# Performance work log

Hardware: AMD Instinct MI355X
Metric: run time of the kernel (lower is better)

Reference implementation:

```python
import jax, jax.numpy as jnp
import numpy as np

ALIBI_SLOPES = jnp.array([0.6299605249, 0.396850263, 0.25, 0.1574901312,
                          0.0992125657, 0.0625, 0.0393725328, 0.0248031414,
                          0.015625, 0.0098431332, 0.0062007854, 0.00390625],
                         dtype=jnp.float32)
H, D = 12, 64
SCALE = D ** (-0.5)


def setup_inputs() -> dict:
    key = jax.random.key(0)
    ks = jax.random.split(key, 9)
    B, S, E = 4, 2048, 768
    s = 0.02
    return {
        "x": jax.random.normal(ks[0], (B, S, E), dtype=jnp.float32),
        "Wq": jax.random.normal(ks[1], (E, E), dtype=jnp.float32) * s,
        "bq": jnp.zeros((E,), dtype=jnp.float32),
        "Wk": jax.random.normal(ks[2], (E, E), dtype=jnp.float32) * s,
        "bk": jnp.zeros((E,), dtype=jnp.float32),
        "Wv": jax.random.normal(ks[3], (E, E), dtype=jnp.float32) * s,
        "bv": jnp.zeros((E,), dtype=jnp.float32),
        "Wo": jax.random.normal(ks[4], (E, E), dtype=jnp.float32) * s,
        "bo": jnp.zeros((E,), dtype=jnp.float32),
    }


def reference(x, Wq, bq, Wk, bk, Wv, bv, Wo, bo):
    B, S, E = x.shape
    # projections (weights stored input-major: y = x @ W + b)
    q = (x @ Wq + bq).reshape(B, S, H, D).transpose(0, 2, 1, 3)  # [B,H,S,D]
    k = (x @ Wk + bk).reshape(B, S, H, D).transpose(0, 2, 1, 3)
    v = (x @ Wv + bv).reshape(B, S, H, D).transpose(0, 2, 1, 3)

    scores = jnp.einsum('bhqd,bhkd->bhqk', q, k) * SCALE  # [B,H,S,S]

    pos = jnp.arange(S, dtype=jnp.float32)
    a = ALIBI_SLOPES[:, None] * pos[None, :]          # [H,S]
    alibi = a[:, :, None] - a[:, None, :]             # [H,S,S]
    scores = scores + alibi[None]

    causal = jnp.triu(jnp.ones((S, S), dtype=bool), k=1)  # True above diag
    scores = jnp.where(causal[None, None], -jnp.inf, scores)

    attn = jax.nn.softmax(scores, axis=-1)
    o = jnp.einsum('bhqk,bhkd->bhqd', attn, v)  # [B,H,S,D]

    # Faithful to original: view of contiguous (B,H,S,D) buffer as (B,S,E)
    # (head-major flatten, reproducing the original module's reshape).
    o = o.reshape(B, S, E)
    return o @ Wo + bo
```

## Files before the change

### kernel.cpp

```cpp
#include <hip/hip_runtime.h>
#include <hip/hip_bf16.h>
#include <cstdint>
#include <cstddef>

#define B_ 4
#define S_ 2048
#define E_ 768
#define H_ 12
#define D_ 64

typedef __bf16 bf16x8 __attribute__((ext_vector_type(8)));
typedef float f32x4 __attribute__((ext_vector_type(4)));

__constant__ float c_slopes[12] = {
    0.6299605249f, 0.396850263f, 0.25f, 0.1574901312f,
    0.0992125657f, 0.0625f, 0.0393725328f, 0.0248031414f,
    0.015625f, 0.0098431332f, 0.0062007854f, 0.00390625f};

__device__ __forceinline__ unsigned short f2bf_u(float f) {
    unsigned u = __builtin_bit_cast(unsigned, f);
    u += 0x7fffu + ((u >> 16) & 1u);
    return (unsigned short)(u >> 16);
}
__device__ __forceinline__ __bf16 f2bf(float f) {
    unsigned short s = f2bf_u(f);
    return __builtin_bit_cast(__bf16, s);
}

__device__ __forceinline__ void gload_lds16(const void* g, void* l) {
    __builtin_amdgcn_global_load_lds(
        (const __attribute__((address_space(1))) unsigned int*)g,
        (__attribute__((address_space(3))) unsigned int*)l, 16, 0, 0);
}

__global__ __launch_bounds__(256) void cvt_x(const float* __restrict__ src,
                                             __bf16* __restrict__ dst) {
    int i = (blockIdx.x * 256 + threadIdx.x) * 4;
    float4 v = *(const float4*)(src + i);
    ushort4 o;
    o.x = f2bf_u(v.x); o.y = f2bf_u(v.y); o.z = f2bf_u(v.z); o.w = f2bf_u(v.w);
    *(ushort4*)((unsigned short*)dst + i) = o;
}

__global__ __launch_bounds__(256) void wtrans(const float* __restrict__ W0,
                                              const float* __restrict__ W1,
                                              const float* __restrict__ W2,
                                              const float* __restrict__ W3,
                                              __bf16* __restrict__ Wt) {
    const float* W = blockIdx.z == 0 ? W0 : blockIdx.z == 1 ? W1
                   : blockIdx.z == 2 ? W2 : W3;
    __bf16* out = Wt + (size_t)blockIdx.z * E_ * E_;
    __shared__ alignas(16) __bf16 ts[64 * 72];
    const int t = threadIdx.x;
    const int k0 = blockIdx.y * 64, n0 = blockIdx.x * 64;
#pragma unroll
    for (int i = 0; i < 4; i++) {
        int idx = i * 256 + t;
        int row = idx >> 4, c4 = idx & 15;
        float4 v = *(const float4*)(W + (size_t)(k0 + row) * E_ + n0 + c4 * 4);
        ts[(c4 * 4 + 0) * 72 + row] = f2bf(v.x);
        ts[(c4 * 4 + 1) * 72 + row] = f2bf(v.y);
        ts[(c4 * 4 + 2) * 72 + row] = f2bf(v.z);
        ts[(c4 * 4 + 3) * 72 + row] = f2bf(v.w);
    }
    __syncthreads();
#pragma unroll
    for (int i = 0; i < 2; i++) {
        int idx = i * 256 + t;
        int r = idx >> 3, c8 = idx & 7;
        *(uint4*)((unsigned short*)out + (size_t)(n0 + r) * E_ + k0 + c8 * 8) =
            *(const uint4*)((const unsigned short*)ts + r * 72 + c8 * 8);
    }
}

__global__ __launch_bounds__(256, 3) void qkv_gemm(
    const __bf16* __restrict__ A, const __bf16* __restrict__ WtAll,
    const float* __restrict__ b0, const float* __restrict__ b1,
    const float* __restrict__ b2, __bf16* __restrict__ Qb,
    __bf16* __restrict__ Kb, __bf16* __restrict__ Vtb) {
    constexpr int Kd = E_;
    __shared__ alignas(16) __bf16 Asm[2][128 * 32];
    __shared__ alignas(16) __bf16 Bsm[2][3][64 * 32];

    const int t = threadIdx.x;
    const int w = t >> 6, lane = t & 63;
    const int qm = lane & 15, quad = lane >> 4;
    const int m0 = blockIdx.y * 128, n0 = blockIdx.x * 64;
    const int wm = w * 32;

    float bvv[3][4];
    const float* bs[3] = {b0, b1, b2};
#pragma unroll
    for (int z = 0; z < 3; z++)
#pragma unroll
        for (int j = 0; j < 4; j++) bvv[z][j] = bs[z][n0 + j * 16 + qm];

    const int crow = lane >> 2;
    const int ccol = lane & 3;

    f32x4 acc[3][2][4] = {};

    for (int k0 = 0; k0 < Kd; k0 += 64) {
#pragma unroll
        for (int p = 0; p < 2; p++) {
            const int kp = k0 + p * 32;
#pragma unroll
            for (int cc = 0; cc < 2; cc++) {
                int chunk = w * 2 + cc;
                gload_lds16((const unsigned short*)A +
                                (size_t)(m0 + chunk * 16 + crow) * Kd + kp + ccol * 8,
                            Asm[p] + chunk * 512);
            }
#pragma unroll
            for (int e = 0; e < 3; e++) {
                int g = w * 3 + e;
                int z = g >> 2, cz = g & 3;
                gload_lds16((const unsigned short*)WtAll + (size_t)z * Kd * E_ +
                                (size_t)(n0 + cz * 16 + crow) * Kd + kp + ccol * 8,
                            Bsm[p][z] + cz * 512);
            }
        }
        __syncthreads();

#pragma unroll
        for (int p = 0; p < 2; p++) {
            bf16x8 af[2];
#pragma unroll
            for (int i = 0; i < 2; i++)
                af[i] = *(const bf16x8*)(Asm[p] + (wm + i * 16 + qm) * 32 + quad * 8);
#pragma unroll
            for (int z = 0; z < 3; z++) {
                bf16x8 bg[4];
#pragma unroll
                for (int j = 0; j < 4; j++)
                    bg[j] = *(const bf16x8*)(Bsm[p][z] + (j * 16 + qm) * 32 + quad * 8);
#pragma unroll
                for (int i = 0; i < 2; i++)
#pragma unroll
                    for (int j = 0; j < 4; j++)
                        acc[z][i][j] = __builtin_amdgcn_mfma_f32_16x16x32_bf16(
                            af[i], bg[j], acc[z][i][j], 0, 0, 0);
            }
        }
        __syncthreads();
    }

#pragma unroll
    for (int z = 0; z < 3; z++) {
        __bf16* out = z == 0 ? Qb : z == 1 ? Kb : Vtb;
#pragma unroll
        for (int i = 0; i < 2; i++) {
#pragma unroll
            for (int j = 0; j < 4; j++) {
                int col = n0 + j * 16 + qm;
                int rowb = m0 + wm + i * 16 + quad * 4;
                int h = col >> 6, d = col & (D_ - 1);
                if (z == 2) {
                    int b = rowb >> 11, s = rowb & (S_ - 1);
                    unsigned short pk4[4];
#pragma unroll
                    for (int r = 0; r < 4; r++)
                        pk4[r] = f2bf_u(acc[z][i][j][r] + bvv[z][j]);
                    uint2 pv;
                    pv.x = (unsigned)pk4[0] | ((unsigned)pk4[1] << 16);
                    pv.y = (unsigned)pk4[2] | ((unsigned)pk4[3] << 16);
                    *(uint2*)((unsigned short*)out +
                              ((size_t)(b * H_ + h) * D_ + d) * S_ + s) = pv;
                } else {
#pragma unroll
                    for (int r = 0; r < 4; r++) {
                        int row = rowb + r;
                        int b = row >> 11, s = row & (S_ - 1);
                        out[(((size_t)(b * H_ + h)) * S_ + s) * D_ + d] =
                            f2bf(acc[z][i][j][r] + bvv[z][j]);
                    }
                }
            }
        }
    }
}

__global__ __launch_bounds__(256) void gemm_out(
    const __bf16* __restrict__ A, const __bf16* __restrict__ Wt,
    const float* __restrict__ bias, float* __restrict__ outF) {
    constexpr int Kd = E_, N = E_;
    __shared__ alignas(16) __bf16 Asm[2][128 * 32];
    __shared__ alignas(16) __bf16 Bsm[2][128 * 32];

    const int t = threadIdx.x;
    const int w = t >> 6, lane = t & 63;
    const int qm = lane & 15, quad = lane >> 4;
    const int m0 = blockIdx.y * 128, n0 = blockIdx.x * 128;
    const int wm = (w >> 1) * 64, wn = (w & 1) * 64;

    float bvv[4];
#pragma unroll
    for (int j = 0; j < 4; j++) bvv[j] = bias[n0 + wn + j * 16 + qm];

    const int crow = lane >> 2;
    const int ccol = lane & 3;

    f32x4 acc[4][4] = {};

    for (int k0 = 0; k0 < Kd; k0 += 64) {
#pragma unroll
        for (int p = 0; p < 2; p++) {
            const int kp = k0 + p * 32;
#pragma unroll
            for (int cc = 0; cc < 2; cc++) {
                int chunk = w * 2 + cc;
                int row = chunk * 16 + crow;
                gload_lds16((const unsigned short*)A + (size_t)(m0 + row) * Kd + kp + ccol * 8,
                            Asm[p] + chunk * 512);
                gload_lds16((const unsigned short*)Wt + (size_t)(n0 + row) * Kd + kp + ccol * 8,
                            Bsm[p] + chunk * 512);
            }
        }
        __syncthreads();

#pragma unroll
        for (int p = 0; p < 2; p++) {
            bf16x8 af[4], bg[4];
#pragma unroll
            for (int i = 0; i < 4; i++)
                af[i] = *(const bf16x8*)(Asm[p] + (wm + i * 16 + qm) * 32 + quad * 8);
#pragma unroll
            for (int j = 0; j < 4; j++)
                bg[j] = *(const bf16x8*)(Bsm[p] + (wn + j * 16 + qm) * 32 + quad * 8);
#pragma unroll
            for (int i = 0; i < 4; i++)
#pragma unroll
                for (int j = 0; j < 4; j++)
                    acc[i][j] = __builtin_amdgcn_mfma_f32_16x16x32_bf16(
                        af[i], bg[j], acc[i][j], 0, 0, 0);
        }
        __syncthreads();
    }

#pragma unroll
    for (int i = 0; i < 4; i++) {
#pragma unroll
        for (int j = 0; j < 4; j++) {
            int col = n0 + wn + j * 16 + qm;
            int rowb = m0 + wm + i * 16 + quad * 4;
#pragma unroll
            for (int r = 0; r < 4; r++) {
                int row = rowb + r;
                outF[(size_t)row * N + col] = acc[i][j][r] + bvv[j];
            }
        }
    }
}

__global__ __launch_bounds__(256, 6) void attn_k(
    const __bf16* __restrict__ Q, const __bf16* __restrict__ K,
    const __bf16* __restrict__ Vt, __bf16* __restrict__ O) {
    __shared__ alignas(16) __bf16 Ksm[2][64 * 32];
    __shared__ alignas(16) __bf16 Vsm[2][64 * 32];
    __shared__ alignas(16) __bf16 Psm[4 * 16 * 64];

    const int t = threadIdx.x;
    const int w = t >> 6, lane = t & 63;
    const int qm = lane & 15, quad = lane >> 4;
    const int L = blockIdx.x;
    const int r = L & 7;
    const int m = (L >> 3) & 31;
    const int s = L >> 8;
    const int bh = r * 6 + s;
    const int qt = (m + s * 5 + (s >> 1)) & 31;
    const float c2 = c_slopes[bh % H_] * 1.44269504f;
    const size_t base = (size_t)bh * S_ * D_;

    const int bb = qt * 64 + w * 16;
    const __bf16* qp = Q + base + (size_t)(bb + qm) * D_ + quad * 8;
    bf16x8 qf0 = *(const bf16x8*)qp;
    bf16x8 qf1 = *(const bf16x8*)(qp + 32);

    f32x4 oacc[4] = {};
    float lsum = 0.f;
    char* Pb = (char*)Psm + w * 2048;

    const int srow = lane >> 2;
    const int sq = (lane & 3) ^ ((lane >> 3) & 3);
    const unsigned short* Kg = (const unsigned short*)K + base +
                               (size_t)(16 * w + srow) * D_ + sq * 8;
    const unsigned short* Vg = (const unsigned short*)Vt + base +
                               (size_t)(16 * w + srow) * S_ + sq * 8;

    const int cq = (quad ^ ((qm >> 1) & 3)) * 8;
    const int pf = (qm & 7) << 4;

    for (int kt = 0; kt <= qt; kt++) {
#pragma unroll
        for (int h = 0; h < 2; h++) {
            gload_lds16(Kg + (size_t)(kt * 64) * D_ + 32 * h, Ksm[h] + w * 512);
            gload_lds16(Vg + kt * 64 + 32 * h, Vsm[h] + w * 512);
        }
        __syncthreads();

        bf16x8 ak[4][2], bv[4][2];
#pragma unroll
        for (int i = 0; i < 4; i++) {
            ak[i][0] = *(const bf16x8*)(Ksm[0] + (16 * i + qm) * 32 + cq);
            ak[i][1] = *(const bf16x8*)(Ksm[1] + (16 * i + qm) * 32 + cq);
        }
#pragma unroll
        for (int jd = 0; jd < 4; jd++) {
            bv[jd][0] = *(const bf16x8*)(Vsm[0] + (16 * jd + qm) * 32 + cq);
            bv[jd][1] = *(const bf16x8*)(Vsm[1] + (16 * jd + qm) * 32 + cq);
        }

        f32x4 st[4];
#pragma unroll
        for (int i = 0; i < 4; i++) {
            f32x4 zz = {0.f, 0.f, 0.f, 0.f};
            zz = __builtin_amdgcn_mfma_f32_16x16x32_bf16(ak[i][0], qf0, zz, 0, 0, 0);
            zz = __builtin_amdgcn_mfma_f32_16x16x32_bf16(ak[i][1], qf1, zz, 0, 0, 0);
            st[i] = zz;
        }

        const int qi = bb + qm;
        const bool nomask = (kt * 64 + 63) <= bb;
        float ls = 0.f;
        unsigned pk[4][2];
#pragma unroll
        for (int i = 0; i < 4; i++) {
            float bi = -c2 * (float)(kt * 64 + 16 * i + 4 * quad);
            float p[4];
#pragma unroll
            for (int rr = 0; rr < 4; rr++) {
                float tt = st[i][rr] * 0.18033688f + (bi - c2 * (float)rr);
                float pp = __builtin_amdgcn_exp2f(tt);
                if (!nomask) {
                    int key = kt * 64 + 16 * i + 4 * quad + rr;
                    pp = (key > qi) ? 0.f : pp;
                }
                ls += pp;
                p[rr] = pp;
            }
            unsigned u0 = __builtin_bit_cast(unsigned, p[0]) + 0x8000u;
            unsigned u1 = __builtin_bit_cast(unsigned, p[1]) + 0x8000u;
            unsigned u2 = __builtin_bit_cast(unsigned, p[2]) + 0x8000u;
            unsigned u3 = __builtin_bit_cast(unsigned, p[3]) + 0x8000u;
            pk[i][0] = __builtin_amdgcn_perm(u1, u0, 0x07060302u);
            pk[i][1] = __builtin_amdgcn_perm(u3, u2, 0x07060302u);
        }
        lsum += ls;

#pragma unroll
        for (int i = 0; i < 4; i++) {
            uint2 pv; pv.x = pk[i][0]; pv.y = pk[i][1];
            *(uint2*)(Pb + qm * 128 + ((32 * i + 8 * quad) ^ pf)) = pv;
        }

        bf16x8 ap0 = *(const bf16x8*)(Pb + qm * 128 + ((quad * 16) ^ pf));
        bf16x8 ap1 = *(const bf16x8*)(Pb + qm * 128 + ((64 + quad * 16) ^ pf));
#pragma unroll
        for (int jd = 0; jd < 4; jd++) {
            oacc[jd] = __builtin_amdgcn_mfma_f32_16x16x32_bf16(
                ap0, bv[jd][0], oacc[jd], 0, 0, 0);
            oacc[jd] = __builtin_amdgcn_mfma_f32_16x16x32_bf16(
                ap1, bv[jd][1], oacc[jd], 0, 0, 0);
        }

        __syncthreads();
    }

    float lf = lsum;
    lf += __shfl_xor(lf, 16);
    lf += __shfl_xor(lf, 32);
#pragma unroll
    for (int rr = 0; rr < 4; rr++) {
        float lr = __shfl(lf, 4 * quad + rr);
        float inv = 1.0f / lr;
        int qrow = bb + 4 * quad + rr;
#pragma unroll
        for (int jd = 0; jd < 4; jd++)
            O[base + (size_t)qrow * D_ + 16 * jd + qm] =
                f2bf(oacc[jd][rr] * inv);
    }
}

extern "C" void kernel_launch(void* const* d_in, const int* in_sizes, int n_in,
                              void* d_out, int out_size, void* d_ws, size_t ws_size,
                              hipStream_t stream) {
    (void)in_sizes; (void)n_in; (void)out_size; (void)ws_size;
    const float* x  = (const float*)d_in[0];
    const float* Wq = (const float*)d_in[1];
    const float* bq = (const float*)d_in[2];
    const float* Wk = (const float*)d_in[3];
    const float* bk = (const float*)d_in[4];
    const float* Wv = (const float*)d_in[5];
    const float* bv = (const float*)d_in[6];
    const float* Wo = (const float*)d_in[7];
    const float* bo = (const float*)d_in[8];
    float* out = (float*)d_out;

    const size_t n = (size_t)B_ * H_ * S_ * D_;
    __bf16* xb  = (__bf16*)d_ws;
    __bf16* Qb  = xb + n;
    __bf16* Kb  = xb + 2 * n;
    __bf16* Vtb = xb + 3 * n;
    __bf16* Wt  = xb + 4 * n;
    __bf16* Ob  = Qb;

    cvt_x<<<6144, 256, 0, stream>>>(x, xb);
    wtrans<<<dim3(12, 12, 4), 256, 0, stream>>>(Wq, Wk, Wv, Wo, Wt);
    qkv_gemm<<<dim3(12, 64), 256, 0, stream>>>(
        xb, Wt, bq, bk, bv, Qb, Kb, Vtb);
    attn_k<<<1536, 256, 0, stream>>>(Qb, Kb, Vtb, Ob);
    gemm_out<<<dim3(6, 64), 256, 0, stream>>>(
        Ob, Wt + 3 * (size_t)E_ * E_, bo, out);
}
```

Measured before the change: 218.8 us.

## Merge input conversion kernels and shrink output GEMM tile to 128x64

Folds the x-to-bf16 conversion and weight transpose into one launch, dispatching on block index, which removes one kernel launch and the gap between the two. The output projection GEMM moves from 128x128 to 128x64 tiles, doubling the grid from 384 to 768 blocks and adding an occupancy hint, to fill more of the GPU's compute units. Smaller tiles reuse less data per block and reload the A operand more often.

```diff
diff --git a/kernel.cpp b/kernel.cpp
--- a/kernel.cpp
+++ b/kernel.cpp
@@ -33,26 +33,27 @@
         (__attribute__((address_space(3))) unsigned int*)l, 16, 0, 0);
 }
 
-__global__ __launch_bounds__(256) void cvt_x(const float* __restrict__ src,
-                                             __bf16* __restrict__ dst) {
-    int i = (blockIdx.x * 256 + threadIdx.x) * 4;
-    float4 v = *(const float4*)(src + i);
-    ushort4 o;
-    o.x = f2bf_u(v.x); o.y = f2bf_u(v.y); o.z = f2bf_u(v.z); o.w = f2bf_u(v.w);
-    *(ushort4*)((unsigned short*)dst + i) = o;
-}
-
-__global__ __launch_bounds__(256) void wtrans(const float* __restrict__ W0,
-                                              const float* __restrict__ W1,
-                                              const float* __restrict__ W2,
-                                              const float* __restrict__ W3,
-                                              __bf16* __restrict__ Wt) {
-    const float* W = blockIdx.z == 0 ? W0 : blockIdx.z == 1 ? W1
-                   : blockIdx.z == 2 ? W2 : W3;
-    __bf16* out = Wt + (size_t)blockIdx.z * E_ * E_;
+__global__ __launch_bounds__(256) void prep(
+    const float* __restrict__ x, __bf16* __restrict__ xb,
+    const float* __restrict__ W0, const float* __restrict__ W1,
+    const float* __restrict__ W2, const float* __restrict__ W3,
+    __bf16* __restrict__ Wt) {
     __shared__ alignas(16) __bf16 ts[64 * 72];
+    const int L = blockIdx.x;
     const int t = threadIdx.x;
-    const int k0 = blockIdx.y * 64, n0 = blockIdx.x * 64;
+    if (L < 6144) {
+        int i = (L * 256 + t) * 4;
+        float4 v = *(const float4*)(x + i);
+        ushort4 o;
+        o.x = f2bf_u(v.x); o.y = f2bf_u(v.y); o.z = f2bf_u(v.z); o.w = f2bf_u(v.w);
+        *(ushort4*)((unsigned short*)xb + i) = o;
+        return;
+    }
+    const int id = L - 6144;
+    const int z = id / 144, rem = id % 144;
+    const int k0 = (rem / 12) * 64, n0 = (rem % 12) * 64;
+    const float* W = z == 0 ? W0 : z == 1 ? W1 : z == 2 ? W2 : W3;
+    __bf16* out = Wt + (size_t)z * E_ * E_;
 #pragma unroll
     for (int i = 0; i < 4; i++) {
         int idx = i * 256 + t;
@@ -180,27 +181,27 @@
     }
 }
 
-__global__ __launch_bounds__(256) void gemm_out(
+__global__ __launch_bounds__(256, 3) void gemm_out(
     const __bf16* __restrict__ A, const __bf16* __restrict__ Wt,
     const float* __restrict__ bias, float* __restrict__ outF) {
     constexpr int Kd = E_, N = E_;
     __shared__ alignas(16) __bf16 Asm[2][128 * 32];
-    __shared__ alignas(16) __bf16 Bsm[2][128 * 32];
+    __shared__ alignas(16) __bf16 Bsm[2][64 * 32];
 
     const int t = threadIdx.x;
     const int w = t >> 6, lane = t & 63;
     const int qm = lane & 15, quad = lane >> 4;
-    const int m0 = blockIdx.y * 128, n0 = blockIdx.x * 128;
-    const int wm = (w >> 1) * 64, wn = (w & 1) * 64;
+    const int m0 = blockIdx.y * 128, n0 = blockIdx.x * 64;
+    const int wm = w * 32;
 
     float bvv[4];
 #pragma unroll
-    for (int j = 0; j < 4; j++) bvv[j] = bias[n0 + wn + j * 16 + qm];
+    for (int j = 0; j < 4; j++) bvv[j] = bias[n0 + j * 16 + qm];
 
     const int crow = lane >> 2;
     const int ccol = lane & 3;
 
-    f32x4 acc[4][4] = {};
+    f32x4 acc[2][4] = {};
 
     for (int k0 = 0; k0 < Kd; k0 += 64) {
 #pragma unroll
@@ -209,26 +210,27 @@
 #pragma unroll
             for (int cc = 0; cc < 2; cc++) {
                 int chunk = w * 2 + cc;
-                int row = chunk * 16 + crow;
-                gload_lds16((const unsigned short*)A + (size_t)(m0 + row) * Kd + kp + ccol * 8,
+                gload_lds16((const unsigned short*)A +
+                                (size_t)(m0 + chunk * 16 + crow) * Kd + kp + ccol * 8,
                             Asm[p] + chunk * 512);
-                gload_lds16((const unsigned short*)Wt + (size_t)(n0 + row) * Kd + kp + ccol * 8,
-                            Bsm[p] + chunk * 512);
-            }
+            }
+            gload_lds16((const unsigned short*)Wt +
+                            (size_t)(n0 + w * 16 + crow) * Kd + kp + ccol * 8,
+                        Bsm[p] + w * 512);
         }
         __syncthreads();
 
 #pragma unroll
         for (int p = 0; p < 2; p++) {
-            bf16x8 af[4], bg[4];
-#pragma unroll
-            for (int i = 0; i < 4; i++)
+            bf16x8 af[2], bg[4];
+#pragma unroll
+            for (int i = 0; i < 2; i++)
                 af[i] = *(const bf16x8*)(Asm[p] + (wm + i * 16 + qm) * 32 + quad * 8);
 #pragma unroll
             for (int j = 0; j < 4; j++)
-                bg[j] = *(const bf16x8*)(Bsm[p] + (wn + j * 16 + qm) * 32 + quad * 8);
-#pragma unroll
-            for (int i = 0; i < 4; i++)
+                bg[j] = *(const bf16x8*)(Bsm[p] + (j * 16 + qm) * 32 + quad * 8);
+#pragma unroll
+            for (int i = 0; i < 2; i++)
 #pragma unroll
                 for (int j = 0; j < 4; j++)
                     acc[i][j] = __builtin_amdgcn_mfma_f32_16x16x32_bf16(
@@ -238,16 +240,14 @@
     }
 
 #pragma unroll
-    for (int i = 0; i < 4; i++) {
+    for (int i = 0; i < 2; i++) {
 #pragma unroll
         for (int j = 0; j < 4; j++) {
-            int col = n0 + wn + j * 16 + qm;
+            int col = n0 + j * 16 + qm;
             int rowb = m0 + wm + i * 16 + quad * 4;
 #pragma unroll
-            for (int r = 0; r < 4; r++) {
-                int row = rowb + r;
-                outF[(size_t)row * N + col] = acc[i][j][r] + bvv[j];
-            }
+            for (int r = 0; r < 4; r++)
+                outF[(size_t)(rowb + r) * N + col] = acc[i][j][r] + bvv[j];
         }
     }
 }
@@ -404,11 +404,10 @@
     __bf16* Wt  = xb + 4 * n;
     __bf16* Ob  = Qb;
 
-    cvt_x<<<6144, 256, 0, stream>>>(x, xb);
-    wtrans<<<dim3(12, 12, 4), 256, 0, stream>>>(Wq, Wk, Wv, Wo, Wt);
+    prep<<<6720, 256, 0, stream>>>(x, xb, Wq, Wk, Wv, Wo, Wt);
     qkv_gemm<<<dim3(12, 64), 256, 0, stream>>>(
         xb, Wt, bq, bk, bv, Qb, Kb, Vtb);
     attn_k<<<1536, 256, 0, stream>>>(Qb, Kb, Vtb, Ob);
-    gemm_out<<<dim3(6, 64), 256, 0, stream>>>(
+    gemm_out<<<dim3(12, 64), 256, 0, stream>>>(
         Ob, Wt + 3 * (size_t)E_ * E_, bo, out);
 }
```

Result: no change. 218.7 us (-0.0%).
